# Kernel optimization log

Measured on AMD Instinct MI355X. Metric: run time of the kernel, lower is better.

## Reference

```python
import jax, jax.numpy as jnp
import numpy as np

HEAD_SIZE = 64

def setup_inputs() -> dict:
    key = jax.random.key(0)
    ks = jax.random.split(key, 6)
    B, T, D, H, HS = 4, 2048, 1024, 16, HEAD_SIZE
    s = 1.0 / np.sqrt(D)
    return {
        "x": jax.random.normal(ks[0], (B, T, D), jnp.float32),
        "Wq": jax.random.normal(ks[1], (H, D, HS), jnp.float32) * s,
        "Wk": jax.random.normal(ks[2], (H, D, HS), jnp.float32) * s,
        "Wv": jax.random.normal(ks[3], (H, D, HS), jnp.float32) * s,
        "Wp": jax.random.normal(ks[4], (D, D), jnp.float32) * s,
        "bp": jnp.zeros((D,), jnp.float32),
    }

def reference(x, Wq, Wk, Wv, Wp, bp):
    B, T, D = x.shape
    H, _, HS = Wq.shape
    # per-head projections (bias-free Linears), stacked over heads
    q = jnp.einsum('btd,hde->bhte', x, Wq)
    k = jnp.einsum('btd,hde->bhte', x, Wk)
    v = jnp.einsum('btd,hde->bhte', x, Wv)
    scores = jnp.einsum('bhqe,bhke->bhqk', q, k) / jnp.sqrt(jnp.float32(HS))
    causal = jnp.tril(jnp.ones((T, T), bool))  # mask[:T,:T]
    scores = jnp.where(causal, scores, -jnp.inf)
    w = jax.nn.softmax(scores, axis=-1)  # dropout p=0.0 -> identity
    out = jnp.einsum('bhqk,bhke->bhqe', w, v)
    # concat heads along last dim: [B,T,H*HS] == [B,T,D]
    out = out.transpose(0, 2, 1, 3).reshape(B, T, H * HS)
    return out @ Wp.T + bp  # note: Wp stored as [out,in] like nn.Linear
```

## Files before the change

### kernel.cpp

```cpp
#include <hip/hip_runtime.h>
#include <hip/hip_bf16.h>

typedef unsigned short u16;
typedef unsigned int u32;
typedef __attribute__((ext_vector_type(8))) short short8;
typedef __attribute__((ext_vector_type(4))) float f32x4;

#define B_ 4
#define T_ 2048
#define D_ 1024
#define H_ 16
#define HS_ 64
#define BT (B_*T_)

__device__ __forceinline__ float bf2f(u16 b){ union{u32 u; float f;} v; v.u=((u32)b)<<16; return v.f; }
__device__ __forceinline__ u16 f2bf(float f){
    __hip_bfloat16 h = __float2bfloat16(f);
    union{__hip_bfloat16 h; u16 u;} v; v.h = h; return v.u;
}
__device__ __forceinline__ void split2(float x, u16& h, u16& l){
    u16 hb = f2bf(x);
    float fh = bf2f(hb);
    h = hb; l = f2bf(x - fh);
}
union U4 { u16 s[4]; uint2 v; };
union S8 { u16 s[8]; short8 v; };

#define GLD16(g,l) __builtin_amdgcn_global_load_lds( \
    (__attribute__((address_space(1))) void*)(u16*)(g), \
    (__attribute__((address_space(3))) void*)(l), 16, 0, 0)

__device__ __forceinline__ int swz(int row, int col){
    return row*64 + (((col>>3) ^ (row&7))<<3) + (col&7);
}
#define FCHK(r) (((r)>>1)&3)

__global__ __launch_bounds__(256) void pack_w(const float* __restrict__ Wq,
                                              const float* __restrict__ Wk,
                                              const float* __restrict__ Wv,
                                              u16* __restrict__ Wth,
                                              u16* __restrict__ Wtl)
{
    __shared__ float Tl[64*68];
    const int h = blockIdx.x, dt = blockIdx.y, z = blockIdx.z;
    const float* src = (z==0) ? Wq : ((z==1) ? Wk : Wv);
    const int t = threadIdx.x;
    const int d0 = dt*64;
    #pragma unroll
    for (int i=0;i<4;++i){
        int ci = t + 256*i;
        int dr = ci>>4, ec = ci&15;
        float4 v = *(const float4*)(src + ((size_t)h*D_ + d0+dr)*HS_ + ec*4);
        *(float4*)(Tl + dr*68 + ec*4) = v;
    }
    __syncthreads();
    #pragma unroll
    for (int i=0;i<4;++i){
        int ci = t + 256*i;
        int e = ci>>4, dc = ci&15;
        U4 hh, ll;
        #pragma unroll
        for (int j=0;j<4;++j){
            float f = Tl[(dc*4+j)*68 + e];
            split2(f, hh.s[j], ll.s[j]);
        }
        int n = z*D_ + h*HS_ + e;
        *(uint2*)(Wth + (size_t)n*D_ + d0 + dc*4) = hh.v;
        *(uint2*)(Wtl + (size_t)n*D_ + d0 + dc*4) = ll.v;
    }
}

__global__ __launch_bounds__(256) void gemm_qkv(const float* __restrict__ x,
                                                const u16* __restrict__ Wth,
                                                const u16* __restrict__ Wtl,
                                                float* __restrict__ qo,
                                                u16* __restrict__ kho, u16* __restrict__ klo,
                                                u16* __restrict__ vth, u16* __restrict__ vtl)
{
    __shared__ u16 Ash[128*32], Asl[128*32];
    __shared__ u16 Bsh[128*32], Bsl[128*32];
    const int n0 = blockIdx.x*128, m0 = blockIdx.y*128;
    const int t = threadIdx.x;
    const int w = t>>6, lane = t&63, quad = lane>>4, l16 = lane&15;
    const int wm = (w>>1)*64, wn = (w&1)*64;
    f32x4 acc[4][4];
    #pragma unroll
    for (int i=0;i<4;++i)
        #pragma unroll
        for (int j=0;j<4;++j) acc[i][j] = (f32x4){0.f,0.f,0.f,0.f};
    for (int kt=0; kt<32; ++kt){
        const int k0 = kt*32;
        #pragma unroll
        for (int i=0;i<2;++i){
            int ci = t + 256*i;
            int row = ci>>2, c = ci&3;
            int cs = c ^ FCHK(row);
            GLD16(Wth + (size_t)(n0+row)*D_ + k0 + cs*8, Bsh + ci*8);
            GLD16(Wtl + (size_t)(n0+row)*D_ + k0 + cs*8, Bsl + ci*8);
        }
        #pragma unroll
        for (int i=0;i<4;++i){
            int ci = t + 256*i;
            int row = ci>>3, c4 = ci&7;
            float4 av = *(const float4*)(x + (size_t)(m0+row)*D_ + k0 + c4*4);
            U4 hh, ll;
            split2(av.x, hh.s[0], ll.s[0]); split2(av.y, hh.s[1], ll.s[1]);
            split2(av.z, hh.s[2], ll.s[2]); split2(av.w, hh.s[3], ll.s[3]);
            int off = row*32 + ((((c4>>1) ^ FCHK(row))<<3) | ((c4&1)<<2));
            *(uint2*)(Ash + off) = hh.v;
            *(uint2*)(Asl + off) = ll.v;
        }
        __syncthreads();
        short8 afh[4], afl[4], bfh[4], bfl[4];
        #pragma unroll
        for (int mi=0;mi<4;++mi){
            const int rr = wm+mi*16+l16;
            const int off = rr*32 + ((quad ^ FCHK(rr))<<3);
            afh[mi] = *(const short8*)(Ash + off);
            afl[mi] = *(const short8*)(Asl + off);
        }
        #pragma unroll
        for (int ni=0;ni<4;++ni){
            const int rr = wn+ni*16+l16;
            const int off = rr*32 + ((quad ^ FCHK(rr))<<3);
            bfh[ni] = *(const short8*)(Bsh + off);
            bfl[ni] = *(const short8*)(Bsl + off);
        }
        #pragma unroll
        for (int mi=0;mi<4;++mi)
            #pragma unroll
            for (int ni=0;ni<4;++ni){
                acc[mi][ni] = __builtin_amdgcn_mfma_f32_16x16x32_bf16(afh[mi], bfh[ni], acc[mi][ni], 0,0,0);
                acc[mi][ni] = __builtin_amdgcn_mfma_f32_16x16x32_bf16(afh[mi], bfl[ni], acc[mi][ni], 0,0,0);
                acc[mi][ni] = __builtin_amdgcn_mfma_f32_16x16x32_bf16(afl[mi], bfh[ni], acc[mi][ni], 0,0,0);
            }
        __syncthreads();
    }
    const int z = n0 >> 10;
    if (z == 0){
        #pragma unroll
        for (int ni=0;ni<4;++ni){
            const int nloc = (n0 & 1023) + wn + ni*16 + l16;
            #pragma unroll
            for (int mi=0;mi<4;++mi){
                const int row = m0 + wm + mi*16 + quad*4;
                #pragma unroll
                for (int r=0;r<4;++r)
                    qo[(size_t)(row+r)*D_ + nloc] = acc[mi][ni][r];
            }
        }
    } else if (z == 1){
        #pragma unroll
        for (int ni=0;ni<4;++ni){
            const int nloc = (n0 & 1023) + wn + ni*16 + l16;
            #pragma unroll
            for (int mi=0;mi<4;++mi){
                const int row = m0 + wm + mi*16 + quad*4;
                #pragma unroll
                for (int r=0;r<4;++r){
                    u16 hh, ll; split2(acc[mi][ni][r], hh, ll);
                    kho[(size_t)(row+r)*D_ + nloc] = hh;
                    klo[(size_t)(row+r)*D_ + nloc] = ll;
                }
            }
        }
    } else {
        #pragma unroll
        for (int ni=0;ni<4;++ni){
            const int nloc = (n0 & 1023) + wn + ni*16 + l16;
            const int hloc = nloc>>6, e = nloc&63;
            #pragma unroll
            for (int mi=0;mi<4;++mi){
                const int rowb = m0 + wm + mi*16 + quad*4;
                const int bidx = rowb >> 11, tloc = rowb & 2047;
                U4 hh, ll;
                #pragma unroll
                for (int r=0;r<4;++r) split2(acc[mi][ni][r], hh.s[r], ll.s[r]);
                const size_t adr = ((size_t)((bidx*16 + hloc)*64 + e))*T_ + tloc;
                *(uint2*)(vth + adr) = hh.v;
                *(uint2*)(vtl + adr) = ll.v;
            }
        }
    }
}

__global__ __launch_bounds__(512, 2) void attn(const float* __restrict__ qf,
                                            const u16* __restrict__ kh, const u16* __restrict__ kl,
                                            const u16* __restrict__ vth, const u16* __restrict__ vtl,
                                            float* __restrict__ att)
{
    __shared__ u16 KshH[2*64*64], KshL[2*64*64];
    __shared__ u16 VshH[2*64*64], VshL[2*64*64];
    __shared__ u16 Pb[8*16*64];
    const int x = blockIdx.y & 7;
    const int bh = (blockIdx.x << 3) | (blockIdx.y >> 3);
    const int b = bh >> 4, h = bh & 15;
    const int t = threadIdx.x;
    const int w = t>>6, lane = t&63, quad = lane>>4, l16 = lane&15;

    u16* Pm = Pb + w*1024;

    const int srow = t>>3;
    const int csrc = (t&7) ^ (srow&7);
    const int ldst = t*8;

    #define STAGE_KV(kvbase, bsel) do{                                         \
        const size_t gk_ = ((size_t)(b*T_ + (kvbase) + srow))*D_ + h*64 + csrc*8; \
        GLD16(kh  + gk_, KshH + (bsel)*4096 + ldst);                           \
        GLD16(kl  + gk_, KshL + (bsel)*4096 + ldst);                           \
        const size_t gv_ = ((size_t)(bh*64 + srow))*T_ + (kvbase) + csrc*8;    \
        GLD16(vth + gv_, VshH + (bsel)*4096 + ldst);                           \
        GLD16(vtl + gv_, VshL + (bsel)*4096 + ldst);                           \
    }while(0)

    int cur = 0;
    STAGE_KV(0, 0);

    #pragma unroll 1
    for (int seg=0; seg<2; ++seg){
        const int qi = seg ? x : (15 - x);
        const int qrow = qi*128 + w*16;
        const int q_abs = qrow + l16;

        short8 qh_[2], ql_[2];
        {
            const float* qp = qf + ((size_t)(b*T_ + qrow + l16))*D_ + h*64;
            #pragma unroll
            for (int ks=0;ks<2;++ks){
                float4 a0 = *(const float4*)(qp + ks*32 + quad*8);
                float4 a1 = *(const float4*)(qp + ks*32 + quad*8 + 4);
                S8 hh, ll;
                split2(a0.x, hh.s[0], ll.s[0]); split2(a0.y, hh.s[1], ll.s[1]);
                split2(a0.z, hh.s[2], ll.s[2]); split2(a0.w, hh.s[3], ll.s[3]);
                split2(a1.x, hh.s[4], ll.s[4]); split2(a1.y, hh.s[5], ll.s[5]);
                split2(a1.z, hh.s[6], ll.s[6]); split2(a1.w, hh.s[7], ll.s[7]);
                qh_[ks] = hh.v; ql_[ks] = ll.v;
            }
        }
        f32x4 o[4];
        #pragma unroll
        for (int i=0;i<4;++i) o[i] = (f32x4){0.f,0.f,0.f,0.f};
        float m_i = -INFINITY, l_i = 0.f;

        const int kvT = 2*qi + 2;
        for (int kvt=0; kvt<kvT; ++kvt){
            __syncthreads();
            const int nk = (kvt+1 < kvT) ? (kvt+1) : ((seg==0) ? 0 : -1);
            if (nk >= 0) STAGE_KV(nk*64, cur^1);

            const u16* KH = KshH + cur*4096;
            const u16* KL = KshL + cur*4096;
            const u16* VH = VshH + cur*4096;
            const u16* VL = VshL + cur*4096;

            float s[4][4];
            __builtin_amdgcn_s_setprio(1);
            #pragma unroll
            for (int ni=0;ni<4;++ni){
                f32x4 sa = (f32x4){0.f,0.f,0.f,0.f};
                const int row = ni*16 + l16;
                #pragma unroll
                for (int ks=0;ks<2;++ks){
                    const int co = swz(row, ks*32 + quad*8);
                    short8 k8h = *(const short8*)(KH + co);
                    short8 k8l = *(const short8*)(KL + co);
                    sa = __builtin_amdgcn_mfma_f32_16x16x32_bf16(k8h, qh_[ks], sa, 0,0,0);
                    sa = __builtin_amdgcn_mfma_f32_16x16x32_bf16(k8l, qh_[ks], sa, 0,0,0);
                    sa = __builtin_amdgcn_mfma_f32_16x16x32_bf16(k8h, ql_[ks], sa, 0,0,0);
                }
                #pragma unroll
                for (int r=0;r<4;++r) s[ni][r] = sa[r]*0.125f;
            }
            __builtin_amdgcn_s_setprio(0);
            if (kvt*64 + 63 > qrow){
                #pragma unroll
                for (int ni=0;ni<4;++ni){
                    #pragma unroll
                    for (int r=0;r<4;++r){
                        const int kv_abs = kvt*64 + ni*16 + quad*4 + r;
                        if (kv_abs > q_abs) s[ni][r] = -INFINITY;
                    }
                }
            }
            float rm = s[0][0];
            #pragma unroll
            for (int ni=0;ni<4;++ni)
                #pragma unroll
                for (int r=0;r<4;++r) rm = fmaxf(rm, s[ni][r]);
            rm = fmaxf(rm, __shfl_xor(rm, 16));
            rm = fmaxf(rm, __shfl_xor(rm, 32));
            const float mnew = fmaxf(m_i, rm);
            const float alpha = __expf(m_i - mnew);
            m_i = mnew;
            float rs = 0.f;
            #pragma unroll
            for (int ni=0;ni<4;++ni)
                #pragma unroll
                for (int r=0;r<4;++r){
                    s[ni][r] = __expf(s[ni][r] - mnew);
                    rs += s[ni][r];
                }
            rs += __shfl_xor(rs, 16);
            rs += __shfl_xor(rs, 32);
            l_i = l_i*alpha + rs;
            float a4[4];
            #pragma unroll
            for (int r=0;r<4;++r) a4[r] = __shfl(alpha, quad*4 + r);
            #pragma unroll
            for (int ni=0;ni<4;++ni)
                #pragma unroll
                for (int r=0;r<4;++r) o[ni][r] *= a4[r];

            uint2 plv[4];
            #pragma unroll
            for (int ni=0;ni<4;++ni){
                U4 hh, ll;
                #pragma unroll
                for (int r=0;r<4;++r) split2(s[ni][r], hh.s[r], ll.s[r]);
                *(uint2*)(Pm + swz(l16, ni*16 + quad*4)) = hh.v;
                plv[ni] = ll.v;
            }
            __asm__ volatile("s_waitcnt lgkmcnt(0)" ::: "memory");
            short8 pah[2], pal[2];
            #pragma unroll
            for (int ks=0;ks<2;++ks)
                pah[ks] = *(const short8*)(Pm + swz(l16, ks*32 + quad*8));
            __asm__ volatile("" ::: "memory");
            #pragma unroll
            for (int ni=0;ni<4;++ni)
                *(uint2*)(Pm + swz(l16, ni*16 + quad*4)) = plv[ni];
            __asm__ volatile("s_waitcnt lgkmcnt(0)" ::: "memory");
            #pragma unroll
            for (int ks=0;ks<2;++ks)
                pal[ks] = *(const short8*)(Pm + swz(l16, ks*32 + quad*8));
            __asm__ volatile("" ::: "memory");

            __builtin_amdgcn_s_setprio(1);
            #pragma unroll
            for (int ni=0;ni<4;++ni){
                const int row = ni*16 + l16;
                #pragma unroll
                for (int ks=0;ks<2;++ks){
                    const int co = swz(row, ks*32 + quad*8);
                    short8 v8h = *(const short8*)(VH + co);
                    short8 v8l = *(const short8*)(VL + co);
                    o[ni] = __builtin_amdgcn_mfma_f32_16x16x32_bf16(pah[ks], v8h, o[ni], 0,0,0);
                    o[ni] = __builtin_amdgcn_mfma_f32_16x16x32_bf16(pah[ks], v8l, o[ni], 0,0,0);
                    o[ni] = __builtin_amdgcn_mfma_f32_16x16x32_bf16(pal[ks], v8h, o[ni], 0,0,0);
                }
            }
            __builtin_amdgcn_s_setprio(0);
            cur ^= 1;
        }
        float lt[4];
        #pragma unroll
        for (int r=0;r<4;++r) lt[r] = __shfl(l_i, quad*4 + r);
        const size_t ob = (size_t)(b*T_ + qrow);
        #pragma unroll
        for (int ni=0;ni<4;++ni){
            const int col = h*64 + ni*16 + l16;
            #pragma unroll
            for (int r=0;r<4;++r)
                att[(ob + quad*4 + r)*D_ + col] = o[ni][r] / lt[r];
        }
    }
    #undef STAGE_KV
}

__global__ __launch_bounds__(256) void gemm_bt(const float* __restrict__ A,
                                               const float* __restrict__ Bt,
                                               float* __restrict__ C,
                                               const float* __restrict__ bias,
                                               int M, int N, int K)
{
    __shared__ u16 Ash[128*32], Asl[128*32];
    __shared__ u16 Bsh[128*32], Bsl[128*32];
    const int n0 = blockIdx.x*128, m0 = blockIdx.y*128;
    const int t = threadIdx.x;
    const int w = t>>6, lane = t&63, quad = lane>>4, l16 = lane&15;
    const int wm = (w>>1)*64, wn = (w&1)*64;
    f32x4 acc[4][4];
    #pragma unroll
    for (int i=0;i<4;++i)
        #pragma unroll
        for (int j=0;j<4;++j) acc[i][j] = (f32x4){0.f,0.f,0.f,0.f};
    const int kT = K >> 5;
    for (int kt=0; kt<kT; ++kt){
        const int k0 = kt*32;
        #pragma unroll
        for (int i=0;i<4;++i){
            int ci = t + 256*i;
            int row = ci>>3, c4 = ci&7;
            float4 av = *(const float4*)(A  + (size_t)(m0+row)*K + k0 + c4*4);
            float4 bv = *(const float4*)(Bt + (size_t)(n0+row)*K + k0 + c4*4);
            U4 ah, al, bh, bl;
            split2(av.x, ah.s[0], al.s[0]); split2(av.y, ah.s[1], al.s[1]);
            split2(av.z, ah.s[2], al.s[2]); split2(av.w, ah.s[3], al.s[3]);
            split2(bv.x, bh.s[0], bl.s[0]); split2(bv.y, bh.s[1], bl.s[1]);
            split2(bv.z, bh.s[2], bl.s[2]); split2(bv.w, bh.s[3], bl.s[3]);
            int off = row*32 + ((((c4>>1) ^ FCHK(row))<<3) | ((c4&1)<<2));
            *(uint2*)(Ash + off) = ah.v;
            *(uint2*)(Asl + off) = al.v;
            *(uint2*)(Bsh + off) = bh.v;
            *(uint2*)(Bsl + off) = bl.v;
        }
        __syncthreads();
        short8 afh[4], afl[4], bfh[4], bfl[4];
        #pragma unroll
        for (int mi=0;mi<4;++mi){
            const int rr = wm+mi*16+l16;
            const int off = rr*32 + ((quad ^ FCHK(rr))<<3);
            afh[mi] = *(const short8*)(Ash + off);
            afl[mi] = *(const short8*)(Asl + off);
        }
        #pragma unroll
        for (int ni=0;ni<4;++ni){
            const int rr = wn+ni*16+l16;
            const int off = rr*32 + ((quad ^ FCHK(rr))<<3);
            bfh[ni] = *(const short8*)(Bsh + off);
            bfl[ni] = *(const short8*)(Bsl + off);
        }
        #pragma unroll
        for (int mi=0;mi<4;++mi)
            #pragma unroll
            for (int ni=0;ni<4;++ni){
                acc[mi][ni] = __builtin_amdgcn_mfma_f32_16x16x32_bf16(afh[mi], bfh[ni], acc[mi][ni], 0,0,0);
                acc[mi][ni] = __builtin_amdgcn_mfma_f32_16x16x32_bf16(afh[mi], bfl[ni], acc[mi][ni], 0,0,0);
                acc[mi][ni] = __builtin_amdgcn_mfma_f32_16x16x32_bf16(afl[mi], bfh[ni], acc[mi][ni], 0,0,0);
            }
        __syncthreads();
    }
    #pragma unroll
    for (int ni=0;ni<4;++ni){
        const int col = n0 + wn + ni*16 + l16;
        const float bv = bias ? bias[col] : 0.f;
        #pragma unroll
        for (int mi=0;mi<4;++mi){
            const int row = m0 + wm + mi*16 + quad*4;
            #pragma unroll
            for (int r=0;r<4;++r)
                C[(size_t)(row+r)*N + col] = acc[mi][ni][r] + bv;
        }
    }
}

extern "C" void kernel_launch(void* const* d_in, const int* in_sizes, int n_in,
                              void* d_out, int out_size, void* d_ws, size_t ws_size,
                              hipStream_t stream)
{
    const float* x  = (const float*)d_in[0];
    const float* Wq = (const float*)d_in[1];
    const float* Wk = (const float*)d_in[2];
    const float* Wv = (const float*)d_in[3];
    const float* Wp = (const float*)d_in[4];
    const float* bp = (const float*)d_in[5];
    float* out = (float*)d_out;

    float* q   = (float*)d_ws;
    u16*  kh   = (u16*)(q + (size_t)BT*D_);
    u16*  kl   = kh + (size_t)BT*D_;
    u16*  vth  = kl + (size_t)BT*D_;
    u16*  vtl  = vth + (size_t)BT*D_;
    float* att = (float*)(vtl + (size_t)BT*D_);
    u16*  Wth  = (u16*)att;
    u16*  Wtl  = Wth + (size_t)3072*D_;

    pack_w  <<<dim3(16,16,3), 256, 0, stream>>>(Wq, Wk, Wv, Wth, Wtl);
    gemm_qkv<<<dim3(24, BT/128), 256, 0, stream>>>(x, Wth, Wtl, q, kh, kl, vth, vtl);
    attn    <<<dim3(8, 64), 512, 0, stream>>>(q, kh, kl, vth, vtl, att);
    gemm_bt <<<dim3(8, BT/128), 256, 0, stream>>>(att, Wp, out, bp, BT, D_, D_);
}
```

Before: 469.3 us.

## Process both paired query tiles in one KV sweep to share K/V staging

Before, each block handled two causal query tiles (15-x and x) one after the other, streaming K/V separately for each. Now both tiles' Q fragments and accumulators live in registers together. A single pass over the longer tile's KV range feeds both tiles, and the shorter one stops when its causal range ends. This removes the duplicate global-to-LDS K/V loads and barriers for the shorter tile, but doubles Q and accumulator register use, which may lower occupancy or cause spills.

```diff
diff --git a/kernel.cpp b/kernel.cpp
--- a/kernel.cpp
+++ b/kernel.cpp
@@ -216,43 +216,59 @@
     int cur = 0;
     STAGE_KV(0, 0);
 
-    #pragma unroll 1
-    for (int seg=0; seg<2; ++seg){
-        const int qi = seg ? x : (15 - x);
-        const int qrow = qi*128 + w*16;
-        const int q_abs = qrow + l16;
-
-        short8 qh_[2], ql_[2];
-        {
-            const float* qp = qf + ((size_t)(b*T_ + qrow + l16))*D_ + h*64;
-            #pragma unroll
-            for (int ks=0;ks<2;++ks){
-                float4 a0 = *(const float4*)(qp + ks*32 + quad*8);
-                float4 a1 = *(const float4*)(qp + ks*32 + quad*8 + 4);
-                S8 hh, ll;
-                split2(a0.x, hh.s[0], ll.s[0]); split2(a0.y, hh.s[1], ll.s[1]);
-                split2(a0.z, hh.s[2], ll.s[2]); split2(a0.w, hh.s[3], ll.s[3]);
-                split2(a1.x, hh.s[4], ll.s[4]); split2(a1.y, hh.s[5], ll.s[5]);
-                split2(a1.z, hh.s[6], ll.s[6]); split2(a1.w, hh.s[7], ll.s[7]);
-                qh_[ks] = hh.v; ql_[ks] = ll.v;
-            }
-        }
-        f32x4 o[4];
-        #pragma unroll
-        for (int i=0;i<4;++i) o[i] = (f32x4){0.f,0.f,0.f,0.f};
-        float m_i = -INFINITY, l_i = 0.f;
-
-        const int kvT = 2*qi + 2;
-        for (int kvt=0; kvt<kvT; ++kvt){
-            __syncthreads();
-            const int nk = (kvt+1 < kvT) ? (kvt+1) : ((seg==0) ? 0 : -1);
-            if (nk >= 0) STAGE_KV(nk*64, cur^1);
-
-            const u16* KH = KshH + cur*4096;
-            const u16* KL = KshL + cur*4096;
-            const u16* VH = VshH + cur*4096;
-            const u16* VL = VshL + cur*4096;
-
+    const int qiA = 15 - x, qiB = x;
+    const int qrowA = qiA*128 + w*16, qrowB = qiB*128 + w*16;
+    const int qA_abs = qrowA + l16,   qB_abs = qrowB + l16;
+
+    short8 qAh[2], qAl[2], qBh[2], qBl[2];
+    {
+        const float* qp = qf + ((size_t)(b*T_ + qrowA + l16))*D_ + h*64;
+        #pragma unroll
+        for (int ks=0;ks<2;++ks){
+            float4 a0 = *(const float4*)(qp + ks*32 + quad*8);
+            float4 a1 = *(const float4*)(qp + ks*32 + quad*8 + 4);
+            S8 hh, ll;
+            split2(a0.x, hh.s[0], ll.s[0]); split2(a0.y, hh.s[1], ll.s[1]);
+            split2(a0.z, hh.s[2], ll.s[2]); split2(a0.w, hh.s[3], ll.s[3]);
+            split2(a1.x, hh.s[4], ll.s[4]); split2(a1.y, hh.s[5], ll.s[5]);
+            split2(a1.z, hh.s[6], ll.s[6]); split2(a1.w, hh.s[7], ll.s[7]);
+            qAh[ks] = hh.v; qAl[ks] = ll.v;
+        }
+    }
+    {
+        const float* qp = qf + ((size_t)(b*T_ + qrowB + l16))*D_ + h*64;
+        #pragma unroll
+        for (int ks=0;ks<2;++ks){
+            float4 a0 = *(const float4*)(qp + ks*32 + quad*8);
+            float4 a1 = *(const float4*)(qp + ks*32 + quad*8 + 4);
+            S8 hh, ll;
+            split2(a0.x, hh.s[0], ll.s[0]); split2(a0.y, hh.s[1], ll.s[1]);
+            split2(a0.z, hh.s[2], ll.s[2]); split2(a0.w, hh.s[3], ll.s[3]);
+            split2(a1.x, hh.s[4], ll.s[4]); split2(a1.y, hh.s[5], ll.s[5]);
+            split2(a1.z, hh.s[6], ll.s[6]); split2(a1.w, hh.s[7], ll.s[7]);
+            qBh[ks] = hh.v; qBl[ks] = ll.v;
+        }
+    }
+
+    f32x4 oA[4], oB[4];
+    #pragma unroll
+    for (int i=0;i<4;++i){ oA[i] = (f32x4){0.f,0.f,0.f,0.f}; oB[i] = (f32x4){0.f,0.f,0.f,0.f}; }
+    float mA = -INFINITY, lA = 0.f, mB = -INFINITY, lB = 0.f;
+
+    const int kvTA = 2*qiA + 2;
+    const int kvTB = 2*qiB + 2;
+
+    for (int kvt=0; kvt<kvTA; ++kvt){
+        __syncthreads();
+        if (kvt+1 < kvTA) STAGE_KV((kvt+1)*64, cur^1);
+
+        const u16* KH = KshH + cur*4096;
+        const u16* KL = KshL + cur*4096;
+        const u16* VH = VshH + cur*4096;
+        const u16* VL = VshL + cur*4096;
+
+        auto process = [&](const short8* qh_, const short8* ql_,
+                           int qrow, int q_abs, f32x4* o, float& m_i, float& l_i){
             float s[4][4];
             __builtin_amdgcn_s_setprio(1);
             #pragma unroll
@@ -350,21 +366,41 @@
                 }
             }
             __builtin_amdgcn_s_setprio(0);
-            cur ^= 1;
-        }
+        };
+
+        process(qAh, qAl, qrowA, qA_abs, oA, mA, lA);
+        if (kvt < kvTB)
+            process(qBh, qBl, qrowB, qB_abs, oB, mB, lB);
+        cur ^= 1;
+    }
+    #undef STAGE_KV
+
+    {
         float lt[4];
         #pragma unroll
-        for (int r=0;r<4;++r) lt[r] = __shfl(l_i, quad*4 + r);
-        const size_t ob = (size_t)(b*T_ + qrow);
+        for (int r=0;r<4;++r) lt[r] = __shfl(lA, quad*4 + r);
+        const size_t ob = (size_t)(b*T_ + qrowA);
         #pragma unroll
         for (int ni=0;ni<4;++ni){
             const int col = h*64 + ni*16 + l16;
             #pragma unroll
             for (int r=0;r<4;++r)
-                att[(ob + quad*4 + r)*D_ + col] = o[ni][r] / lt[r];
-        }
-    }
-    #undef STAGE_KV
+                att[(ob + quad*4 + r)*D_ + col] = oA[ni][r] / lt[r];
+        }
+    }
+    {
+        float lt[4];
+        #pragma unroll
+        for (int r=0;r<4;++r) lt[r] = __shfl(lB, quad*4 + r);
+        const size_t ob = (size_t)(b*T_ + qrowB);
+        #pragma unroll
+        for (int ni=0;ni<4;++ni){
+            const int col = h*64 + ni*16 + l16;
+            #pragma unroll
+            for (int r=0;r<4;++r)
+                att[(ob + quad*4 + r)*D_ + col] = oB[ni][r] / lt[r];
+        }
+    }
 }
 
 __global__ __launch_bounds__(256) void gemm_bt(const float* __restrict__ A,
```

After: 505.1 us. 7.6% more time.
